# Performance work log

Hardware: AMD Instinct MI355X
Metric: run time of the kernel (lower is better)

Reference implementation:

```python
import jax, jax.numpy as jnp
import numpy as np

N_NODES = 50000
N_EDGES = 800000
D_IN = 64      # entity_embedding_size_in
D_REL = 64     # relation_embedding_size
D_OUT = 64     # entity_embedding_size_out
IN_DIM = 2 * D_IN + D_REL  # 192


def mish(x):
    return x * jnp.tanh(jax.nn.softplus(x))


def setup_inputs() -> dict:
    key = jax.random.key(0)
    k1, k2, k3, k4 = jax.random.split(key, 4)
    triple_features = jax.random.normal(k1, (N_EDGES, IN_DIM), dtype=jnp.float32)
    # row 0: destination node; row 1: unique slot id per edge (guarantees no
    # duplicate sparse indices, so torch's coalesce would be a no-op)
    dst = jax.random.randint(k2, (N_EDGES,), 0, N_NODES)
    slot = jnp.arange(N_EDGES)
    indices = jnp.stack([dst, slot], axis=0).astype(jnp.int64)
    # Kaiming-uniform-ish init for the two linear layers (bias=False)
    bound1 = float(np.sqrt(6.0 / IN_DIM))
    W_triple = jax.random.uniform(k3, (D_OUT, IN_DIM), minval=-bound1, maxval=bound1, dtype=jnp.float32)
    bound2 = float(np.sqrt(6.0 / D_OUT))
    w_att = jax.random.uniform(k4, (1, D_OUT), minval=-bound2, maxval=bound2, dtype=jnp.float32)
    return {
        "triple_features": triple_features,
        "sparse_triple_adjacency_list_indices": indices,
        "W_triple": W_triple,
        "w_att": w_att,
    }


def reference(triple_features, sparse_triple_adjacency_list_indices, W_triple, w_att):
    # dropout is identity in eval mode
    h = triple_features @ W_triple.T                      # [E, D_OUT]
    a = mish(h @ w_att[0])                                # [E]
    dst = sparse_triple_adjacency_list_indices[0]         # [E] destination node
    # segment softmax of attention logits grouped by destination node
    seg_max = jax.ops.segment_max(a, dst, num_segments=N_NODES)  # [N]
    seg_max = jnp.where(jnp.isfinite(seg_max), seg_max, 0.0)
    e = jnp.exp(a - seg_max[dst])                         # [E]
    denom = jax.ops.segment_sum(e, dst, num_segments=N_NODES)    # [N]
    p = e / denom[dst]                                    # [E]
    # attention-weighted scatter-sum aggregation per node
    out = jax.ops.segment_sum(h * p[:, None], dst, num_segments=N_NODES)  # [N, D_OUT]
    return out
```

## Files before the change

kernel.cpp:

```cpp
#include <hip/hip_runtime.h>
#include <hip/hip_bf16.h>
#include <math.h>


typedef __bf16  bf16x8 __attribute__((ext_vector_type(8)));
typedef float   f32x4  __attribute__((ext_vector_type(4)));

#define KDIM 192
#define LDSS 200

__device__ inline unsigned short f2bf(float f) {
    unsigned u = __float_as_uint(f);
    unsigned r = u + 0x7fffu + ((u >> 16) & 1u);
    return (unsigned short)(r >> 16);
}
__device__ inline float bf2f(unsigned short h) {
    return __uint_as_float(((unsigned)h) << 16);
}

__global__ void init_kernel(int* __restrict__ count, int* __restrict__ cursor, int n_nodes,
                            const float* __restrict__ W, unsigned short* __restrict__ wbf, int wn) {
    int i = blockIdx.x * blockDim.x + threadIdx.x;
    int stride = gridDim.x * blockDim.x;
    for (int j = i; j < n_nodes; j += stride) { count[j] = 0; cursor[j] = 0; }
    for (int j = i; j < wn; j += stride) wbf[j] = f2bf(W[j]);
}

__global__ __launch_bounds__(256)
void gemm_att_kernel(const float* __restrict__ X, const unsigned short* __restrict__ wbf,
                     const float* __restrict__ w_att, const int* __restrict__ dst,
                     unsigned short* __restrict__ h_bf, float* __restrict__ a_out,
                     int* __restrict__ count, int E) {
    __shared__ unsigned short lds_x[64 * LDSS];
    const int e0  = blockIdx.x * 64;
    const int tid = threadIdx.x;

    const float4* Xv = (const float4*)(X + (size_t)e0 * KDIM);
    #pragma unroll
    for (int it = 0; it < 12; ++it) {
        int f = it * 256 + tid;
        int e = f / 48;
        int c = f - e * 48;
        float4 v;
        if (e0 + e < E) v = Xv[f];
        else            v = make_float4(0.f, 0.f, 0.f, 0.f);
        unsigned short* p = &lds_x[e * LDSS + c * 4];
        p[0] = f2bf(v.x); p[1] = f2bf(v.y); p[2] = f2bf(v.z); p[3] = f2bf(v.w);
    }
    __syncthreads();

    const int wave  = tid >> 6;
    const int lane  = tid & 63;
    const int n16   = lane & 15;
    const int quad  = lane >> 4;
    const int m0    = wave * 16;

    f32x4 acc[4] = {{0,0,0,0},{0,0,0,0},{0,0,0,0},{0,0,0,0}};
    #pragma unroll
    for (int kk = 0; kk < 6; ++kk) {
        bf16x8 afrag = *(const bf16x8*)&lds_x[(m0 + n16) * LDSS + kk * 32 + quad * 8];
        #pragma unroll
        for (int nt = 0; nt < 4; ++nt) {
            bf16x8 bfrag = *(const bf16x8*)&wbf[(nt * 16 + n16) * KDIM + kk * 32 + quad * 8];
            acc[nt] = __builtin_amdgcn_mfma_f32_16x16x32_bf16(afrag, bfrag, acc[nt], 0, 0, 0);
        }
    }

    float wa[4];
    #pragma unroll
    for (int nt = 0; nt < 4; ++nt) wa[nt] = w_att[nt * 16 + n16];

    float pa[4] = {0.f, 0.f, 0.f, 0.f};
    #pragma unroll
    for (int nt = 0; nt < 4; ++nt) {
        #pragma unroll
        for (int r = 0; r < 4; ++r) {
            int e = e0 + m0 + quad * 4 + r;
            float v = acc[nt][r];
            if (e < E) h_bf[(size_t)e * 64 + nt * 16 + n16] = f2bf(v);
            pa[r] += v * wa[nt];
        }
    }
    #pragma unroll
    for (int r = 0; r < 4; ++r) {
        float s = pa[r];
        s += __shfl_xor(s, 1);
        s += __shfl_xor(s, 2);
        s += __shfl_xor(s, 4);
        s += __shfl_xor(s, 8);
        pa[r] = s;
    }
    if (n16 == 0) {
        #pragma unroll
        for (int r = 0; r < 4; ++r) {
            int e = e0 + m0 + quad * 4 + r;
            if (e >= E) continue;
            float x = pa[r];
            float mv;
            if (x > 15.0f) {
                mv = x;
            } else {
                float ex = expf(x);
                float t  = (1.0f + ex);
                t = t * t;
                mv = x * (t - 1.0f) / (t + 1.0f);
            }
            a_out[e] = mv;
            atomicAdd(&count[dst[e]], 1);
        }
    }
}

__global__ __launch_bounds__(256)
void scan1_kernel(const int* __restrict__ count, int* __restrict__ offsets,
                  int* __restrict__ bsum, int n) {
    __shared__ int tmp[256];
    int i = blockIdx.x * 256 + threadIdx.x;
    int v = (i < n) ? count[i] : 0;
    tmp[threadIdx.x] = v;
    __syncthreads();
    #pragma unroll
    for (int off = 1; off < 256; off <<= 1) {
        int t = (threadIdx.x >= off) ? tmp[threadIdx.x - off] : 0;
        __syncthreads();
        tmp[threadIdx.x] += t;
        __syncthreads();
    }
    if (i < n) offsets[i] = tmp[threadIdx.x] - v;
    if (threadIdx.x == 255) bsum[blockIdx.x] = tmp[255];
}

__global__ __launch_bounds__(256)
void scan2_kernel(int* __restrict__ bsum, int nb) {
    __shared__ int tmp[256];
    int v = (threadIdx.x < nb) ? bsum[threadIdx.x] : 0;
    tmp[threadIdx.x] = v;
    __syncthreads();
    #pragma unroll
    for (int off = 1; off < 256; off <<= 1) {
        int t = (threadIdx.x >= off) ? tmp[threadIdx.x - off] : 0;
        __syncthreads();
        tmp[threadIdx.x] += t;
        __syncthreads();
    }
    if (threadIdx.x < nb) bsum[threadIdx.x] = tmp[threadIdx.x] - v;
}

__global__ __launch_bounds__(256)
void scan3_kernel(int* __restrict__ offsets, const int* __restrict__ bsum, int n, int E) {
    int i = blockIdx.x * 256 + threadIdx.x;
    if (i < n) offsets[i] += bsum[blockIdx.x];
    if (i == 0) offsets[n] = E;
}

__global__ __launch_bounds__(256)
void scatter_kernel(const int* __restrict__ dst, const int* __restrict__ offsets,
                    int* __restrict__ cursor, int* __restrict__ perm, int E) {
    int e = blockIdx.x * 256 + threadIdx.x;
    if (e < E) {
        int d = dst[e];
        int pos = offsets[d] + atomicAdd(&cursor[d], 1);
        perm[pos] = e;
    }
}

__global__ __launch_bounds__(256)
void aggregate_kernel(const unsigned short* __restrict__ h_bf, const float* __restrict__ a,
                      const int* __restrict__ perm, const int* __restrict__ offsets,
                      float* __restrict__ out, int N) {
    int node = (int)((blockIdx.x * (unsigned)blockDim.x + threadIdx.x) >> 6);
    int lane = threadIdx.x & 63;
    if (node >= N) return;
    int start = offsets[node];
    int end   = offsets[node + 1];
    if (start == end) { out[(size_t)node * 64 + lane] = 0.0f; return; }

    float m = -INFINITY;
    for (int i = start + lane; i < end; i += 64) m = fmaxf(m, a[perm[i]]);
    #pragma unroll
    for (int s = 32; s >= 1; s >>= 1) m = fmaxf(m, __shfl_xor(m, s));

    float acc = 0.0f, ssum = 0.0f;
    for (int i = start; i < end; ++i) {
        int e = perm[i];
        float w = __expf(a[e] - m);
        ssum += w;
        acc  += w * bf2f(h_bf[(size_t)e * 64 + lane]);
    }
    out[(size_t)node * 64 + lane] = acc / ssum;
}

extern "C" void kernel_launch(void* const* d_in, const int* in_sizes, int n_in,
                              void* d_out, int out_size, void* d_ws, size_t ws_size,
                              hipStream_t stream) {
    const float* X     = (const float*)d_in[0];
    const int*   idx   = (const int*)d_in[1];
    const float* W     = (const float*)d_in[2];
    const float* w_att = (const float*)d_in[3];

    const int E       = in_sizes[1] / 2;
    const int n_nodes = out_size / 64;
    const int wn      = in_sizes[2];
    const int* dst    = idx;

    char* ws = (char*)d_ws;
    unsigned short* wbf  = (unsigned short*)ws;
    unsigned short* h_bf = (unsigned short*)(ws + 24576);
    size_t off = 24576 + (size_t)E * 64 * 2;
    float* a       = (float*)(ws + off);  off += (size_t)E * 4;
    int*   perm    = (int*)(ws + off);    off += (size_t)E * 4;
    int*   count   = (int*)(ws + off);    off += (size_t)n_nodes * 4;
    int*   cursor  = (int*)(ws + off);    off += (size_t)n_nodes * 4;
    int*   offsets = (int*)(ws + off);    off += (size_t)(n_nodes + 1) * 4;
    int*   bsum    = (int*)(ws + off);

    float* out = (float*)d_out;

    init_kernel<<<256, 256, 0, stream>>>(count, cursor, n_nodes, W, wbf, wn);

    int nblk_gemm = (E + 63) / 64;
    gemm_att_kernel<<<nblk_gemm, 256, 0, stream>>>(X, wbf, w_att, dst, h_bf, a, count, E);

    int nb = (n_nodes + 255) / 256;
    scan1_kernel<<<nb, 256, 0, stream>>>(count, offsets, bsum, n_nodes);
    scan2_kernel<<<1, 256, 0, stream>>>(bsum, nb);
    scan3_kernel<<<nb, 256, 0, stream>>>(offsets, bsum, n_nodes, E);

    scatter_kernel<<<(E + 255) / 256, 256, 0, stream>>>(dst, offsets, cursor, perm, E);

    int nblk_agg = (n_nodes + 3) / 4;
    aggregate_kernel<<<nblk_agg, 256, 0, stream>>>(h_bf, a, perm, offsets, out, n_nodes);
}
```

Baseline: 1.063 ms.

## Merge scans into single-block kernel, seed cursors, pack LDS writes, unroll aggregation

Replaces the three-kernel prefix scan with one 1024-thread single-block scan that also initialises cursor to the offsets. The scatter then needs no offsets lookup, and init no longer zeroes cursor. The GEMM kernel packs its bf16 LDS stores into 8-byte writes and spreads the mish and atomic count across four lanes instead of one. The aggregation loop is unrolled by two with independent accumulators to expose more memory-level parallelism. Each thread of the single-block scan reads about 49 counts sequentially, which may be slower than the parallel multi-block scan.

```diff
diff --git a/kernel.cpp b/kernel.cpp
--- a/kernel.cpp
+++ b/kernel.cpp
@@ -18,11 +18,11 @@
     return __uint_as_float(((unsigned)h) << 16);
 }
 
-__global__ void init_kernel(int* __restrict__ count, int* __restrict__ cursor, int n_nodes,
+__global__ void init_kernel(int* __restrict__ count, int n_nodes,
                             const float* __restrict__ W, unsigned short* __restrict__ wbf, int wn) {
     int i = blockIdx.x * blockDim.x + threadIdx.x;
     int stride = gridDim.x * blockDim.x;
-    for (int j = i; j < n_nodes; j += stride) { count[j] = 0; cursor[j] = 0; }
+    for (int j = i; j < n_nodes; j += stride) count[j] = 0;
     for (int j = i; j < wn; j += stride) wbf[j] = f2bf(W[j]);
 }
 
@@ -44,8 +44,9 @@
         float4 v;
         if (e0 + e < E) v = Xv[f];
         else            v = make_float4(0.f, 0.f, 0.f, 0.f);
-        unsigned short* p = &lds_x[e * LDSS + c * 4];
-        p[0] = f2bf(v.x); p[1] = f2bf(v.y); p[2] = f2bf(v.z); p[3] = f2bf(v.w);
+        unsigned px = ((unsigned)f2bf(v.y) << 16) | (unsigned)f2bf(v.x);
+        unsigned py = ((unsigned)f2bf(v.w) << 16) | (unsigned)f2bf(v.z);
+        *(uint2*)&lds_x[e * LDSS + c * 4] = make_uint2(px, py);
     }
     __syncthreads();
 
@@ -90,12 +91,11 @@
         s += __shfl_xor(s, 8);
         pa[r] = s;
     }
-    if (n16 == 0) {
-        #pragma unroll
-        for (int r = 0; r < 4; ++r) {
-            int e = e0 + m0 + quad * 4 + r;
-            if (e >= E) continue;
-            float x = pa[r];
+    if (n16 < 4) {
+        int r = n16;
+        int e = e0 + m0 + quad * 4 + r;
+        if (e < E) {
+            float x = (r == 0) ? pa[0] : (r == 1) ? pa[1] : (r == 2) ? pa[2] : pa[3];
             float mv;
             if (x > 15.0f) {
                 mv = x;
@@ -111,55 +111,56 @@
     }
 }
 
+__global__ __launch_bounds__(1024)
+void scan_kernel(const int* __restrict__ count, int* __restrict__ offsets,
+                 int* __restrict__ cursor, int n, int E) {
+    __shared__ int wsum[16];
+    const int tid  = threadIdx.x;
+    const int lane = tid & 63;
+    const int wid  = tid >> 6;
+    const int chunk = (n + 1023) >> 10;
+    const int s = tid * chunk;
+    const int e = min(s + chunk, n);
+
+    int sum = 0;
+    for (int i = s; i < e; ++i) sum += count[i];
+
+    int inc = sum;
+    #pragma unroll
+    for (int off = 1; off < 64; off <<= 1) {
+        int t = __shfl_up(inc, off);
+        if (lane >= off) inc += t;
+    }
+    if (lane == 63) wsum[wid] = inc;
+    __syncthreads();
+    if (wid == 0) {
+        int v = (lane < 16) ? wsum[lane] : 0;
+        #pragma unroll
+        for (int off = 1; off < 16; off <<= 1) {
+            int t = __shfl_up(v, off);
+            if (lane >= off) v += t;
+        }
+        if (lane < 16) wsum[lane] = v;
+    }
+    __syncthreads();
+
+    int base = (wid > 0 ? wsum[wid - 1] : 0) + (inc - sum);
+    int run = base;
+    for (int i = s; i < e; ++i) {
+        offsets[i] = run;
+        cursor[i]  = run;
+        run += count[i];
+    }
+    if (tid == 0) offsets[n] = E;
+}
+
 __global__ __launch_bounds__(256)
-void scan1_kernel(const int* __restrict__ count, int* __restrict__ offsets,
-                  int* __restrict__ bsum, int n) {
-    __shared__ int tmp[256];
-    int i = blockIdx.x * 256 + threadIdx.x;
-    int v = (i < n) ? count[i] : 0;
-    tmp[threadIdx.x] = v;
-    __syncthreads();
-    #pragma unroll
-    for (int off = 1; off < 256; off <<= 1) {
-        int t = (threadIdx.x >= off) ? tmp[threadIdx.x - off] : 0;
-        __syncthreads();
-        tmp[threadIdx.x] += t;
-        __syncthreads();
-    }
-    if (i < n) offsets[i] = tmp[threadIdx.x] - v;
-    if (threadIdx.x == 255) bsum[blockIdx.x] = tmp[255];
-}
-
-__global__ __launch_bounds__(256)
-void scan2_kernel(int* __restrict__ bsum, int nb) {
-    __shared__ int tmp[256];
-    int v = (threadIdx.x < nb) ? bsum[threadIdx.x] : 0;
-    tmp[threadIdx.x] = v;
-    __syncthreads();
-    #pragma unroll
-    for (int off = 1; off < 256; off <<= 1) {
-        int t = (threadIdx.x >= off) ? tmp[threadIdx.x - off] : 0;
-        __syncthreads();
-        tmp[threadIdx.x] += t;
-        __syncthreads();
-    }
-    if (threadIdx.x < nb) bsum[threadIdx.x] = tmp[threadIdx.x] - v;
-}
-
-__global__ __launch_bounds__(256)
-void scan3_kernel(int* __restrict__ offsets, const int* __restrict__ bsum, int n, int E) {
-    int i = blockIdx.x * 256 + threadIdx.x;
-    if (i < n) offsets[i] += bsum[blockIdx.x];
-    if (i == 0) offsets[n] = E;
-}
-
-__global__ __launch_bounds__(256)
-void scatter_kernel(const int* __restrict__ dst, const int* __restrict__ offsets,
+void scatter_kernel(const int* __restrict__ dst,
                     int* __restrict__ cursor, int* __restrict__ perm, int E) {
     int e = blockIdx.x * 256 + threadIdx.x;
     if (e < E) {
         int d = dst[e];
-        int pos = offsets[d] + atomicAdd(&cursor[d], 1);
+        int pos = atomicAdd(&cursor[d], 1);
         perm[pos] = e;
     }
 }
@@ -180,14 +181,25 @@
     #pragma unroll
     for (int s = 32; s >= 1; s >>= 1) m = fmaxf(m, __shfl_xor(m, s));
 
-    float acc = 0.0f, ssum = 0.0f;
-    for (int i = start; i < end; ++i) {
-        int e = perm[i];
-        float w = __expf(a[e] - m);
-        ssum += w;
-        acc  += w * bf2f(h_bf[(size_t)e * 64 + lane]);
-    }
-    out[(size_t)node * 64 + lane] = acc / ssum;
+    float acc0 = 0.0f, s0 = 0.0f, acc1 = 0.0f, s1 = 0.0f;
+    int i = start;
+    for (; i + 1 < end; i += 2) {
+        int ea = perm[i];
+        int eb = perm[i + 1];
+        float w0 = __expf(a[ea] - m);
+        float w1 = __expf(a[eb] - m);
+        s0 += w0;
+        s1 += w1;
+        acc0 += w0 * bf2f(h_bf[(size_t)ea * 64 + lane]);
+        acc1 += w1 * bf2f(h_bf[(size_t)eb * 64 + lane]);
+    }
+    if (i < end) {
+        int ea = perm[i];
+        float w0 = __expf(a[ea] - m);
+        s0 += w0;
+        acc0 += w0 * bf2f(h_bf[(size_t)ea * 64 + lane]);
+    }
+    out[(size_t)node * 64 + lane] = (acc0 + acc1) / (s0 + s1);
 }
 
 extern "C" void kernel_launch(void* const* d_in, const int* in_sizes, int n_in,
@@ -212,21 +224,17 @@
     int*   count   = (int*)(ws + off);    off += (size_t)n_nodes * 4;
     int*   cursor  = (int*)(ws + off);    off += (size_t)n_nodes * 4;
     int*   offsets = (int*)(ws + off);    off += (size_t)(n_nodes + 1) * 4;
-    int*   bsum    = (int*)(ws + off);
 
     float* out = (float*)d_out;
 
-    init_kernel<<<256, 256, 0, stream>>>(count, cursor, n_nodes, W, wbf, wn);
+    init_kernel<<<256, 256, 0, stream>>>(count, n_nodes, W, wbf, wn);
 
     int nblk_gemm = (E + 63) / 64;
     gemm_att_kernel<<<nblk_gemm, 256, 0, stream>>>(X, wbf, w_att, dst, h_bf, a, count, E);
 
-    int nb = (n_nodes + 255) / 256;
-    scan1_kernel<<<nb, 256, 0, stream>>>(count, offsets, bsum, n_nodes);
-    scan2_kernel<<<1, 256, 0, stream>>>(bsum, nb);
-    scan3_kernel<<<nb, 256, 0, stream>>>(offsets, bsum, n_nodes, E);
-
-    scatter_kernel<<<(E + 255) / 256, 256, 0, stream>>>(dst, offsets, cursor, perm, E);
+    scan_kernel<<<1, 1024, 0, stream>>>(count, offsets, cursor, n_nodes, E);
+
+    scatter_kernel<<<(E + 255) / 256, 256, 0, stream>>>(dst, cursor, perm, E);
 
     int nblk_agg = (n_nodes + 3) / 4;
     aggregate_kernel<<<nblk_agg, 256, 0, stream>>>(h_bf, a, perm, offsets, out, n_nodes);
```

After: 1.123 ms. +5.6%, slower.
